# Optimization experiments

Measured on AMD Instinct MI355X. Metric: run time of the kernel, lower is better.

## Reference

```python
import jax, jax.numpy as jnp
import numpy as np

N_USER = 100000
N_ITEM = 50000
N = N_USER + N_ITEM  # 150000 nodes
D = 64               # embedding_size
L = 3                # num_layers
E = 2000000          # edges
B = 8192             # batch of (user, item_p, item_n) triples
INT_W, POP_W, TIDE_W = 0.1, 0.1, 0.2


def setup_inputs() -> dict:
    key = jax.random.key(0)
    ks = jax.random.split(key, 10)
    stdv = 1.0 / np.sqrt(D)
    emb_int = jax.random.uniform(ks[0], (N, D), minval=-stdv, maxval=stdv, dtype=jnp.float32)
    emb_pop = jax.random.uniform(ks[1], (N, D), minval=-stdv, maxval=stdv, dtype=jnp.float32)
    q = jax.random.uniform(ks[2], (N_ITEM,), dtype=jnp.float32)
    b = jax.random.uniform(ks[3], (N_ITEM,), dtype=jnp.float32)
    user = jax.random.randint(ks[4], (B, 1), 0, N_USER)
    item_p = jax.random.randint(ks[5], (B, 1), 0, N_ITEM)
    item_n = jax.random.randint(ks[6], (B, 1), 0, N_ITEM)
    mask = jax.random.randint(ks[7], (B, 1), 0, 2).astype(bool)
    edge_src = jax.random.randint(ks[8], (E,), 0, N)
    edge_dst = jax.random.randint(ks[9], (E,), 0, N)
    return {"emb_int": emb_int, "emb_pop": emb_pop, "q": q, "b": b,
            "user": user, "item_p": item_p, "item_n": item_n, "mask": mask,
            "edge_src": edge_src, "edge_dst": edge_dst}


def reference(emb_int, emb_pop, q, b, user, item_p, item_n, mask, edge_src, edge_dst):
    # --- LightGCN symmetric normalization coefficients (per edge) ---
    ones = jnp.ones(edge_src.shape, emb_int.dtype)
    deg_out = jax.ops.segment_sum(ones, edge_src, num_segments=N)
    deg_in = jax.ops.segment_sum(ones, edge_dst, num_segments=N)
    norm = (jax.lax.rsqrt(jnp.maximum(deg_out, 1.0))[edge_src]
            * jax.lax.rsqrt(jnp.maximum(deg_in, 1.0))[edge_dst])  # [E]

    def propagate(e0):
        # L layers of LGConv (gather-scale-scatter), mean over layer outputs incl. layer 0.
        # Dropout is identity in eval mode (training=False).
        acc, h = e0, e0
        for _ in range(L):
            h = jax.ops.segment_sum(h[edge_src] * norm[:, None], edge_dst, num_segments=N)
            acc = acc + h
        return acc / (L + 1)

    f_int = propagate(emb_int)  # [N, D]
    f_pop = propagate(emb_pop)  # [N, D]

    ip = item_p + N_USER  # item node ids
    inn = item_n + N_USER
    u_i, u_p = f_int[user], f_pop[user]          # [B, 1, D]
    pi_i, pi_p = f_int[ip], f_pop[ip]
    ni_i, ni_p = f_int[inn], f_pop[inn]

    p_score_int = jnp.sum(u_i * pi_i, axis=2)    # [B, 1]
    n_score_int = jnp.sum(u_i * ni_i, axis=2)
    p_score_pop = jnp.sum(u_p * pi_p, axis=2)
    n_score_pop = jnp.sum(u_p * ni_p, axis=2)
    p_score_total = p_score_int + p_score_pop
    n_score_total = n_score_int + n_score_pop

    mf = mask.astype(p_score_int.dtype)
    nmf = (~mask).astype(p_score_int.dtype)

    def mask_bpr(p, n, m):
        return -jnp.mean(m * jax.nn.log_sigmoid(p - n))

    def bpr(p, n):
        return -jnp.mean(jax.nn.log_sigmoid(p - n))

    loss_int = mask_bpr(p_score_int, n_score_int, mf)
    loss_pop = mask_bpr(n_score_pop, p_score_pop, mf) - mask_bpr(p_score_pop, n_score_pop, nmf)

    pop_p = jax.nn.softplus(q[item_p]) + jax.nn.softplus(b[item_p])  # [B, 1]
    pop_n = jax.nn.softplus(q[item_n]) + jax.nn.softplus(b[item_n])
    loss_tide = bpr(jnp.tanh(pop_p) * p_score_total, jnp.tanh(pop_n) * n_score_total)

    return INT_W * loss_int + POP_W * loss_pop + TIDE_W * loss_tide
```

## Files before the change

kernel.cpp:

```cpp
#include <hip/hip_runtime.h>
#include <hip/hip_bf16.h>
#include <math.h>

#define N_USER 100000
#define N_ITEM 50000
#define NNODE  150000
#define DIM    64
#define NEDGE  2000000
#define BSZ    8192
#define NTGT   (3*BSZ)
#define CB     586
#define NB     512
#define CH     ((NEDGE + NB - 1)/NB)
#define LBLK   2048
#define PREPB  (NNODE*32/256)
#define CAP    5120

typedef float v2f __attribute__((ext_vector_type(2)));

__device__ __forceinline__ float logsigf(float x){
    return fminf(x, 0.f) - log1pf(expf(-fabsf(x)));
}
__device__ __forceinline__ float softplusf(float x){
    return fmaxf(x, 0.f) + log1pf(expf(-fabsf(x)));
}
__device__ __forceinline__ v2f fp8x2_to_f32(unsigned short u){
    return __builtin_amdgcn_cvt_pk_f32_fp8((int)u, false);
}
__device__ __forceinline__ unsigned short f32_to_fp8x2(float a, float b){
    return (unsigned short)__builtin_amdgcn_cvt_pk_fp8_f32(a, b, 0, false);
}
__device__ __forceinline__ unsigned rfl(unsigned v){
    return (unsigned)__builtin_amdgcn_readfirstlane((int)v);
}

__device__ __forceinline__ void scanCB(unsigned* arr, unsigned* tmp){
    int t = threadIdx.x;
    int base = 3*t;
    unsigned a0=0,a1=0,a2=0;
    if(base   < CB) a0 = arr[base];
    if(base+1 < CB) a1 = arr[base+1];
    if(base+2 < CB) a2 = arr[base+2];
    unsigned s = a0+a1+a2;
    tmp[t]=s; __syncthreads();
    for(int off=1; off<256; off<<=1){
        unsigned v = (t>=off)? tmp[t-off] : 0u;
        __syncthreads();
        tmp[t] += v;
        __syncthreads();
    }
    unsigned excl = tmp[t]-s;
    if(base   < CB) arr[base]   = excl;
    if(base+1 < CB) arr[base+1] = excl+a0;
    if(base+2 < CB) arr[base+2] = excl+a0+a1;
    __syncthreads();
}

__global__ __launch_bounds__(256) void k_hist(const int* __restrict__ src, const int* __restrict__ dst,
                       unsigned* __restrict__ histD, unsigned* __restrict__ histS,
                       const float2* __restrict__ ei, const float2* __restrict__ ep,
                       unsigned* __restrict__ hC32,
                       const unsigned char* __restrict__ mask8, unsigned* __restrict__ mflag){
    if(blockIdx.x >= NB){
        if(blockIdx.x == NB + PREPB){
            __shared__ int any;
            if(threadIdx.x==0) any=0;
            __syncthreads();
            for(int i=threadIdx.x;i<BSZ;i+=256){ if((i&3) && mask8[i]) any=1; }
            __syncthreads();
            if(threadIdx.x==0) *mflag = (any!=0) ? 1u : 0u;
            return;
        }
        int idx = (blockIdx.x - NB)*256 + threadIdx.x;
        int n = idx>>5, c = idx&31;
        float2 va, vb;
        if(c<16){ va = ei[(size_t)n*32 + 2*c]; vb = ei[(size_t)n*32 + 2*c+1]; }
        else    { va = ep[(size_t)n*32 + 2*c-32]; vb = ep[(size_t)n*32 + 2*c-31]; }
        int d = __builtin_amdgcn_cvt_pk_fp8_f32(va.x, va.y, 0, false);
        d = __builtin_amdgcn_cvt_pk_fp8_f32(vb.x, vb.y, d, true);
        hC32[(size_t)n*32 + c] = (unsigned)d;
        return;
    }
    __shared__ unsigned hD[CB], hS[CB];
    for(int i=threadIdx.x;i<CB;i+=256){ hD[i]=0; hS[i]=0; }
    __syncthreads();
    int lo = blockIdx.x*CH, hi = min(lo+CH, NEDGE);
    for(int e=lo+threadIdx.x; e<hi; e+=256){
        atomicAdd(&hS[src[e]>>8],1u);
        atomicAdd(&hD[dst[e]>>8],1u);
    }
    __syncthreads();
    for(int i=threadIdx.x;i<CB;i+=256){
        histD[(size_t)blockIdx.x*CB + i]=hD[i];
        histS[(size_t)blockIdx.x*CB + i]=hS[i];
    }
}

__global__ __launch_bounds__(512) void k_colscan(unsigned* __restrict__ histD, unsigned* __restrict__ histS,
                          unsigned* __restrict__ ctD, unsigned* __restrict__ ctS){
    unsigned* hist = blockIdx.y ? histS : histD;
    unsigned* ct   = blockIdx.y ? ctS   : ctD;
    int b = blockIdx.x;
    __shared__ unsigned sh[512];
    unsigned v = hist[(size_t)threadIdx.x*CB + b];
    sh[threadIdx.x] = v;
    __syncthreads();
    for(int off=1; off<512; off<<=1){
        unsigned t = (threadIdx.x>=off)? sh[threadIdx.x-off] : 0u;
        __syncthreads();
        sh[threadIdx.x] += t;
        __syncthreads();
    }
    hist[(size_t)threadIdx.x*CB + b] = sh[threadIdx.x] - v;
    if(threadIdx.x==511) ct[b] = sh[511];
}

__global__ __launch_bounds__(1024) void k_bstart(const unsigned* __restrict__ ctD, const unsigned* __restrict__ ctS,
                         unsigned* __restrict__ bsD, unsigned* __restrict__ bsS){
    __shared__ unsigned sh[1024];
    unsigned v = (threadIdx.x<CB)? ctD[threadIdx.x] : 0u;
    sh[threadIdx.x]=v; __syncthreads();
    for(int off=1; off<1024; off<<=1){ unsigned t=(threadIdx.x>=off)?sh[threadIdx.x-off]:0u; __syncthreads(); sh[threadIdx.x]+=t; __syncthreads(); }
    if(threadIdx.x<CB) bsD[threadIdx.x]=sh[threadIdx.x]-v;
    if(threadIdx.x==CB-1) bsD[CB]=sh[threadIdx.x];
    __syncthreads();
    unsigned v2 = (threadIdx.x<CB)? ctS[threadIdx.x] : 0u;
    sh[threadIdx.x]=v2; __syncthreads();
    for(int off=1; off<1024; off<<=1){ unsigned t=(threadIdx.x>=off)?sh[threadIdx.x-off]:0u; __syncthreads(); sh[threadIdx.x]+=t; __syncthreads(); }
    if(threadIdx.x<CB) bsS[threadIdx.x]=sh[threadIdx.x]-v2;
    if(threadIdx.x==CB-1) bsS[CB]=sh[threadIdx.x];
}

__global__ __launch_bounds__(256) void k_scatter(const int* __restrict__ src, const int* __restrict__ dst,
                          const unsigned* __restrict__ histD, const unsigned* __restrict__ histS,
                          const unsigned* __restrict__ bsD, const unsigned* __restrict__ bsS,
                          unsigned* __restrict__ part, unsigned char* __restrict__ spart){
    __shared__ unsigned curD[CB], curS[CB];
    __shared__ unsigned lhD[CB], lhS[CB];
    __shared__ unsigned startD[CB], startS[CB];
    __shared__ unsigned tmp[256];
    __shared__ unsigned partl[CH];
    __shared__ unsigned short keyD[CH];
    __shared__ unsigned short keyS[CH];
    __shared__ unsigned char sl[CH];
    for(int i=threadIdx.x;i<CB;i+=256){
        curD[i]=bsD[i]+histD[(size_t)blockIdx.x*CB+i];
        curS[i]=bsS[i]+histS[(size_t)blockIdx.x*CB+i];
        lhD[i]=0; lhS[i]=0;
    }
    __syncthreads();
    int lo=blockIdx.x*CH, hi=min(lo+CH,NEDGE);
    int n = hi-lo;
    for(int e=lo+threadIdx.x;e<hi;e+=256){
        atomicAdd(&lhD[dst[e]>>8],1u);
        atomicAdd(&lhS[src[e]>>8],1u);
    }
    __syncthreads();
    scanCB(lhD, tmp);
    scanCB(lhS, tmp);
    for(int i=threadIdx.x;i<CB;i+=256){ startD[i]=lhD[i]; startS[i]=lhS[i]; }
    __syncthreads();
    for(int e=lo+threadIdx.x;e<hi;e+=256){
        int s=src[e], d=dst[e];
        unsigned bd=(unsigned)(d>>8);
        unsigned slot=atomicAdd(&lhD[bd],1u);
        partl[slot]=((unsigned)(d&255)<<18)|(unsigned)s;
        keyD[slot]=(unsigned short)bd;
        unsigned bs=(unsigned)(s>>8);
        unsigned sslot=atomicAdd(&lhS[bs],1u);
        sl[sslot]=(unsigned char)(s&255);
        keyS[sslot]=(unsigned short)bs;
    }
    __syncthreads();
    for(int k=threadIdx.x;k<n;k+=256){
        unsigned b=keyD[k];
        part[curD[b] + (unsigned)k - startD[b]] = partl[k];
    }
    for(int k=threadIdx.x;k<n;k+=256){
        unsigned b=keyS[k];
        spart[curS[b] + (unsigned)k - startS[b]] = sl[k];
    }
}

__global__ __launch_bounds__(256) void k_degO(const unsigned char* __restrict__ spart, const unsigned* __restrict__ bsS,
                       float* __restrict__ rsqO){
    __shared__ unsigned cnt[256];
    cnt[threadIdx.x]=0;
    __syncthreads();
    unsigned lo=bsS[blockIdx.x], hi=bsS[blockIdx.x+1];
    for(unsigned e=lo+threadIdx.x;e<hi;e+=256) atomicAdd(&cnt[spart[e]],1u);
    __syncthreads();
    int node=(blockIdx.x<<8)+(int)threadIdx.x;
    if(node<NNODE) rsqO[node]=rsqrtf(fmaxf((float)cnt[threadIdx.x],1.f));
}

__global__ __launch_bounds__(256) void k_csr(const unsigned* __restrict__ part, const unsigned* __restrict__ bsD,
                      const float* __restrict__ rsqO,
                      unsigned* __restrict__ rs, unsigned* __restrict__ degI,
                      unsigned* __restrict__ ec){
    __shared__ unsigned cnt[256], cur[256], sh[256];
    __shared__ float rsq[256];
    __shared__ unsigned partl[CAP];
    cnt[threadIdx.x]=0;
    __syncthreads();
    unsigned lo=bsD[blockIdx.x], hi=bsD[blockIdx.x+1];
    unsigned n = hi-lo;
    for(unsigned e=lo+threadIdx.x;e<hi;e+=256) atomicAdd(&cnt[part[e]>>18],1u);
    __syncthreads();
    unsigned c=cnt[threadIdx.x];
    sh[threadIdx.x]=c; __syncthreads();
    for(int o=1;o<256;o<<=1){ unsigned t=(threadIdx.x>=o)?sh[threadIdx.x-o]:0u; __syncthreads(); sh[threadIdx.x]+=t; __syncthreads(); }
    unsigned ex = sh[threadIdx.x]-c;
    rsq[threadIdx.x]=rsqrtf(fmaxf((float)c,1.f));
    cur[threadIdx.x]=ex;
    int node=(blockIdx.x<<8)+(int)threadIdx.x;
    if(node<NNODE){ degI[node]=c; rs[node]=lo+ex; }
    __syncthreads();
    if(n <= CAP){
        for(unsigned e=lo+threadIdx.x;e<hi;e+=256){
            unsigned p=part[e];
            unsigned slot=atomicAdd(&cur[p>>18],1u);
            partl[slot]=p;
        }
        __syncthreads();
        for(unsigned k=threadIdx.x;k<n;k+=256){
            unsigned p=partl[k];
            unsigned fb=p>>18, s=p&0x3FFFFu;
            float w=rsq[fb]*rsqO[s];
            unsigned w14=(unsigned)(w*16383.f + 0.5f);
            ec[lo+k]=(w14<<18)|s;
        }
    } else {
        for(unsigned e=lo+threadIdx.x;e<hi;e+=256){
            unsigned p=part[e];
            unsigned fb=p>>18, s=p&0x3FFFFu;
            unsigned pos=lo+atomicAdd(&cur[fb],1u);
            float w=rsq[fb]*rsqO[s];
            unsigned w14=(unsigned)(w*16383.f + 0.5f);
            ec[pos]=(w14<<18)|s;
        }
    }
}

__device__ __forceinline__ void drain_row(const unsigned short* __restrict__ hin,
                                          const unsigned* __restrict__ ec,
                                          unsigned s, unsigned c, unsigned &i, int lane,
                                          float &ax, float &ay){
    for(; i+4<=c; i+=4){
        unsigned e0=__builtin_nontemporal_load(&ec[s+i]);
        unsigned e1=__builtin_nontemporal_load(&ec[s+i+1]);
        unsigned e2=__builtin_nontemporal_load(&ec[s+i+2]);
        unsigned e3=__builtin_nontemporal_load(&ec[s+i+3]);
        unsigned short u0=hin[(size_t)(e0&0x3FFFFu)*64+lane];
        unsigned short u1=hin[(size_t)(e1&0x3FFFFu)*64+lane];
        unsigned short u2=hin[(size_t)(e2&0x3FFFFu)*64+lane];
        unsigned short u3=hin[(size_t)(e3&0x3FFFFu)*64+lane];
        float w0=(float)(e0>>18)*(1.f/16383.f), w1=(float)(e1>>18)*(1.f/16383.f);
        float w2=(float)(e2>>18)*(1.f/16383.f), w3=(float)(e3>>18)*(1.f/16383.f);
        v2f v;
        v=fp8x2_to_f32(u0); ax+=w0*v.x; ay+=w0*v.y;
        v=fp8x2_to_f32(u1); ax+=w1*v.x; ay+=w1*v.y;
        v=fp8x2_to_f32(u2); ax+=w2*v.x; ay+=w2*v.y;
        v=fp8x2_to_f32(u3); ax+=w3*v.x; ay+=w3*v.y;
    }
    for(; i<c; ++i){
        unsigned e0=__builtin_nontemporal_load(&ec[s+i]);
        unsigned short u0=hin[(size_t)(e0&0x3FFFFu)*64+lane];
        float w0=(float)(e0>>18)*(1.f/16383.f);
        v2f v=fp8x2_to_f32(u0); ax+=w0*v.x; ay+=w0*v.y;
    }
}

__global__ __launch_bounds__(256) void k_spmm_c(const unsigned short* __restrict__ hin, unsigned short* __restrict__ hout,
                                                const unsigned* __restrict__ rs, const unsigned* __restrict__ degI,
                                                const unsigned* __restrict__ ec){
    int wv = (blockIdx.x*256 + threadIdx.x) >> 6;
    int lane = threadIdx.x & 63;
    int r = 4*wv;
    if(r >= NNODE) return;
    unsigned s0=rfl(rs[r  ]), c0=rfl(degI[r  ]);
    unsigned s1=rfl(rs[r+1]), c1=rfl(degI[r+1]);
    unsigned s2=rfl(rs[r+2]), c2=rfl(degI[r+2]);
    unsigned s3=rfl(rs[r+3]), c3=rfl(degI[r+3]);
    float ax0=0,ay0=0, ax1=0,ay1=0, ax2=0,ay2=0, ax3=0,ay3=0;
    unsigned i0=0,i1=0,i2=0,i3=0;
    while(i0+4<=c0 && i1+4<=c1 && i2+4<=c2 && i3+4<=c3){
        unsigned e00=__builtin_nontemporal_load(&ec[s0+i0]);
        unsigned e01=__builtin_nontemporal_load(&ec[s0+i0+1]);
        unsigned e02=__builtin_nontemporal_load(&ec[s0+i0+2]);
        unsigned e03=__builtin_nontemporal_load(&ec[s0+i0+3]);
        unsigned e10=__builtin_nontemporal_load(&ec[s1+i1]);
        unsigned e11=__builtin_nontemporal_load(&ec[s1+i1+1]);
        unsigned e12=__builtin_nontemporal_load(&ec[s1+i1+2]);
        unsigned e13=__builtin_nontemporal_load(&ec[s1+i1+3]);
        unsigned e20=__builtin_nontemporal_load(&ec[s2+i2]);
        unsigned e21=__builtin_nontemporal_load(&ec[s2+i2+1]);
        unsigned e22=__builtin_nontemporal_load(&ec[s2+i2+2]);
        unsigned e23=__builtin_nontemporal_load(&ec[s2+i2+3]);
        unsigned e30=__builtin_nontemporal_load(&ec[s3+i3]);
        unsigned e31=__builtin_nontemporal_load(&ec[s3+i3+1]);
        unsigned e32=__builtin_nontemporal_load(&ec[s3+i3+2]);
        unsigned e33=__builtin_nontemporal_load(&ec[s3+i3+3]);
        unsigned short u00=hin[(size_t)(e00&0x3FFFFu)*64+lane];
        unsigned short u01=hin[(size_t)(e01&0x3FFFFu)*64+lane];
        unsigned short u02=hin[(size_t)(e02&0x3FFFFu)*64+lane];
        unsigned short u03=hin[(size_t)(e03&0x3FFFFu)*64+lane];
        unsigned short u10=hin[(size_t)(e10&0x3FFFFu)*64+lane];
        unsigned short u11=hin[(size_t)(e11&0x3FFFFu)*64+lane];
        unsigned short u12=hin[(size_t)(e12&0x3FFFFu)*64+lane];
        unsigned short u13=hin[(size_t)(e13&0x3FFFFu)*64+lane];
        unsigned short u20=hin[(size_t)(e20&0x3FFFFu)*64+lane];
        unsigned short u21=hin[(size_t)(e21&0x3FFFFu)*64+lane];
        unsigned short u22=hin[(size_t)(e22&0x3FFFFu)*64+lane];
        unsigned short u23=hin[(size_t)(e23&0x3FFFFu)*64+lane];
        unsigned short u30=hin[(size_t)(e30&0x3FFFFu)*64+lane];
        unsigned short u31=hin[(size_t)(e31&0x3FFFFu)*64+lane];
        unsigned short u32v=hin[(size_t)(e32&0x3FFFFu)*64+lane];
        unsigned short u33=hin[(size_t)(e33&0x3FFFFu)*64+lane];
        v2f v; float w;
        v=fp8x2_to_f32(u00); w=(float)(e00>>18)*(1.f/16383.f); ax0+=w*v.x; ay0+=w*v.y;
        v=fp8x2_to_f32(u01); w=(float)(e01>>18)*(1.f/16383.f); ax0+=w*v.x; ay0+=w*v.y;
        v=fp8x2_to_f32(u02); w=(float)(e02>>18)*(1.f/16383.f); ax0+=w*v.x; ay0+=w*v.y;
        v=fp8x2_to_f32(u03); w=(float)(e03>>18)*(1.f/16383.f); ax0+=w*v.x; ay0+=w*v.y;
        v=fp8x2_to_f32(u10); w=(float)(e10>>18)*(1.f/16383.f); ax1+=w*v.x; ay1+=w*v.y;
        v=fp8x2_to_f32(u11); w=(float)(e11>>18)*(1.f/16383.f); ax1+=w*v.x; ay1+=w*v.y;
        v=fp8x2_to_f32(u12); w=(float)(e12>>18)*(1.f/16383.f); ax1+=w*v.x; ay1+=w*v.y;
        v=fp8x2_to_f32(u13); w=(float)(e13>>18)*(1.f/16383.f); ax1+=w*v.x; ay1+=w*v.y;
        v=fp8x2_to_f32(u20); w=(float)(e20>>18)*(1.f/16383.f); ax2+=w*v.x; ay2+=w*v.y;
        v=fp8x2_to_f32(u21); w=(float)(e21>>18)*(1.f/16383.f); ax2+=w*v.x; ay2+=w*v.y;
        v=fp8x2_to_f32(u22); w=(float)(e22>>18)*(1.f/16383.f); ax2+=w*v.x; ay2+=w*v.y;
        v=fp8x2_to_f32(u23); w=(float)(e23>>18)*(1.f/16383.f); ax2+=w*v.x; ay2+=w*v.y;
        v=fp8x2_to_f32(u30); w=(float)(e30>>18)*(1.f/16383.f); ax3+=w*v.x; ay3+=w*v.y;
        v=fp8x2_to_f32(u31); w=(float)(e31>>18)*(1.f/16383.f); ax3+=w*v.x; ay3+=w*v.y;
        v=fp8x2_to_f32(u32v); w=(float)(e32>>18)*(1.f/16383.f); ax3+=w*v.x; ay3+=w*v.y;
        v=fp8x2_to_f32(u33); w=(float)(e33>>18)*(1.f/16383.f); ax3+=w*v.x; ay3+=w*v.y;
        i0+=4; i1+=4; i2+=4; i3+=4;
    }
    drain_row(hin, ec, s0, c0, i0, lane, ax0, ay0);
    drain_row(hin, ec, s1, c1, i1, lane, ax1, ay1);
    drain_row(hin, ec, s2, c2, i2, lane, ax2, ay2);
    drain_row(hin, ec, s3, c3, i3, lane, ax3, ay3);
    hout[(size_t)(r  )*64+lane] = f32_to_fp8x2(ax0, ay0);
    hout[(size_t)(r+1)*64+lane] = f32_to_fp8x2(ax1, ay1);
    hout[(size_t)(r+2)*64+lane] = f32_to_fp8x2(ax2, ay2);
    hout[(size_t)(r+3)*64+lane] = f32_to_fp8x2(ax3, ay3);
}

__global__ __launch_bounds__(256) void k_spmm_t(const unsigned short* __restrict__ hin, float2* __restrict__ h3,
                                                const unsigned* __restrict__ rs, const unsigned* __restrict__ degI,
                                                const unsigned* __restrict__ ec,
                                                const int* __restrict__ user, const int* __restrict__ itp,
                                                const int* __restrict__ itn){
    int wv = (blockIdx.x*256 + threadIdx.x) >> 6;
    int lane = threadIdx.x & 63;
    int t0 = 2*wv, t1 = 2*wv+1;
    if(t0 >= NTGT) return;
    int sec0 = t0>>13, b0 = t0&(BSZ-1);
    int sec1 = t1>>13, b1 = t1&(BSZ-1);
    int n0 = (sec0==0) ? user[b0] : ((sec0==1) ? itp[b0]+N_USER : itn[b0]+N_USER);
    int n1 = (sec1==0) ? user[b1] : ((sec1==1) ? itp[b1]+N_USER : itn[b1]+N_USER);
    n0 = __builtin_amdgcn_readfirstlane(n0);
    n1 = __builtin_amdgcn_readfirstlane(n1);
    unsigned s0 = rfl(rs[n0]), c0 = rfl(degI[n0]);
    unsigned s1 = rfl(rs[n1]), c1 = rfl(degI[n1]);
    float ax0=0.f, ay0=0.f, ax1=0.f, ay1=0.f;
    unsigned i0=0, i1=0;
    while(i0+4<=c0 && i1+4<=c1){
        unsigned e0=ec[s0+i0], e1=ec[s0+i0+1], e2=ec[s0+i0+2], e3=ec[s0+i0+3];
        unsigned e4=ec[s1+i1], e5=ec[s1+i1+1], e6=ec[s1+i1+2], e7=ec[s1+i1+3];
        unsigned short u0=hin[(size_t)(e0&0x3FFFFu)*64+lane];
        unsigned short u1=hin[(size_t)(e1&0x3FFFFu)*64+lane];
        unsigned short u2=hin[(size_t)(e2&0x3FFFFu)*64+lane];
        unsigned short u3=hin[(size_t)(e3&0x3FFFFu)*64+lane];
        unsigned short u4=hin[(size_t)(e4&0x3FFFFu)*64+lane];
        unsigned short u5=hin[(size_t)(e5&0x3FFFFu)*64+lane];
        unsigned short u6=hin[(size_t)(e6&0x3FFFFu)*64+lane];
        unsigned short u7=hin[(size_t)(e7&0x3FFFFu)*64+lane];
        float w0=(float)(e0>>18)*(1.f/16383.f), w1=(float)(e1>>18)*(1.f/16383.f);
        float w2=(float)(e2>>18)*(1.f/16383.f), w3=(float)(e3>>18)*(1.f/16383.f);
        float w4=(float)(e4>>18)*(1.f/16383.f), w5=(float)(e5>>18)*(1.f/16383.f);
        float w6=(float)(e6>>18)*(1.f/16383.f), w7=(float)(e7>>18)*(1.f/16383.f);
        v2f v;
        v=fp8x2_to_f32(u0); ax0+=w0*v.x; ay0+=w0*v.y;
        v=fp8x2_to_f32(u1); ax0+=w1*v.x; ay0+=w1*v.y;
        v=fp8x2_to_f32(u2); ax0+=w2*v.x; ay0+=w2*v.y;
        v=fp8x2_to_f32(u3); ax0+=w3*v.x; ay0+=w3*v.y;
        v=fp8x2_to_f32(u4); ax1+=w4*v.x; ay1+=w4*v.y;
        v=fp8x2_to_f32(u5); ax1+=w5*v.x; ay1+=w5*v.y;
        v=fp8x2_to_f32(u6); ax1+=w6*v.x; ay1+=w6*v.y;
        v=fp8x2_to_f32(u7); ax1+=w7*v.x; ay1+=w7*v.y;
        i0+=4; i1+=4;
    }
    drain_row(hin, ec, s0, c0, i0, lane, ax0, ay0);
    drain_row(hin, ec, s1, c1, i1, lane, ax1, ay1);
    h3[(size_t)t0*64+lane] = make_float2(ax0, ay0);
    h3[(size_t)t1*64+lane] = make_float2(ax1, ay1);
}

__global__ __launch_bounds__(256) void k_scoreloss(const float2* __restrict__ ei, const float2* __restrict__ ep,
                        const unsigned short* __restrict__ h1C, const unsigned short* __restrict__ h2C,
                        const float2* __restrict__ h3,
                        const float* __restrict__ q, const float* __restrict__ bq,
                        const int* __restrict__ user, const int* __restrict__ item_p, const int* __restrict__ item_n,
                        const void* __restrict__ mask, const unsigned* __restrict__ mflag,
                        float4* __restrict__ partial){
    int t = blockIdx.x*256 + threadIdx.x;
    int b = t >> 6, l = t & 63;
    int wv = threadIdx.x >> 6;
    __shared__ float4 wsum[4];
    int nu = user[b];
    int np = item_p[b] + N_USER;
    int nn = item_n[b] + N_USER;

    float2 e0u, e0p, e0n;
    if(l < 32){
        e0u = ei[(size_t)nu*32 + l]; e0p = ei[(size_t)np*32 + l]; e0n = ei[(size_t)nn*32 + l];
    } else {
        e0u = ep[(size_t)nu*32 + (l-32)]; e0p = ep[(size_t)np*32 + (l-32)]; e0n = ep[(size_t)nn*32 + (l-32)];
    }
    v2f h1u = fp8x2_to_f32(h1C[(size_t)nu*64 + l]);
    v2f h1p = fp8x2_to_f32(h1C[(size_t)np*64 + l]);
    v2f h1n = fp8x2_to_f32(h1C[(size_t)nn*64 + l]);
    v2f h2u = fp8x2_to_f32(h2C[(size_t)nu*64 + l]);
    v2f h2p = fp8x2_to_f32(h2C[(size_t)np*64 + l]);
    v2f h2n = fp8x2_to_f32(h2C[(size_t)nn*64 + l]);
    float2 h3u = h3[(size_t)b*64 + l];
    float2 h3p = h3[(size_t)(BSZ   + b)*64 + l];
    float2 h3n = h3[(size_t)(2*BSZ + b)*64 + l];

    float fux = e0u.x + h1u.x + h2u.x + h3u.x, fuy = e0u.y + h1u.y + h2u.y + h3u.y;
    float fpx = e0p.x + h1p.x + h2p.x + h3p.x, fpy = e0p.y + h1p.y + h2p.y + h3p.y;
    float fnx = e0n.x + h1n.x + h2n.x + h3n.x, fny = e0n.y + h1n.y + h2n.y + h3n.y;

    float dp = fux*fpx + fuy*fpy;
    float dn = fux*fnx + fuy*fny;
    for(int off=16; off; off>>=1){ dp += __shfl_down(dp,off,32); dn += __shfl_down(dn,off,32); }
    float pi  = __shfl(dp, 0, 64) * (1.f/16.f);
    float ni  = __shfl(dn, 0, 64) * (1.f/16.f);
    float pp  = __shfl(dp, 32, 64) * (1.f/16.f);
    float npp = __shfl(dn, 32, 64) * (1.f/16.f);
    if(l == 0){
        bool bytes = (*mflag)!=0;
        float mf = bytes ? (((const unsigned char*)mask)[b]?1.f:0.f)
                         : (((const int*)mask)[b]?1.f:0.f);
        float nmf = 1.f-mf;
        float a0 = mf  * logsigf(pi-ni);
        float a1 = mf  * logsigf(npp-pp);
        float a2 = nmf * logsigf(pp-npp);
        int ip=item_p[b], in_=item_n[b];
        float popp = softplusf(q[ip]) + softplusf(bq[ip]);
        float popn = softplusf(q[in_]) + softplusf(bq[in_]);
        float a3 = logsigf(tanhf(popp)*(pi+pp) - tanhf(popn)*(ni+npp));
        wsum[wv] = make_float4(a0,a1,a2,a3);
    }
    __syncthreads();
    if(threadIdx.x == 0){
        float4 s0=wsum[0], s1=wsum[1], s2=wsum[2], s3=wsum[3];
        partial[blockIdx.x] = make_float4(s0.x+s1.x+s2.x+s3.x, s0.y+s1.y+s2.y+s3.y,
                                          s0.z+s1.z+s2.z+s3.z, s0.w+s1.w+s2.w+s3.w);
    }
}

__global__ __launch_bounds__(256) void k_lossfin(const float4* __restrict__ partial, float* __restrict__ out){
    __shared__ float4 sh[256];
    float4 s = make_float4(0,0,0,0);
    for(int i=threadIdx.x; i<LBLK; i+=256){
        float4 v = partial[i];
        s.x+=v.x; s.y+=v.y; s.z+=v.z; s.w+=v.w;
    }
    sh[threadIdx.x]=s;
    __syncthreads();
    for(int off=128; off; off>>=1){
        if(threadIdx.x < off){
            float4 a=sh[threadIdx.x], b2=sh[threadIdx.x+off];
            sh[threadIdx.x]=make_float4(a.x+b2.x,a.y+b2.y,a.z+b2.z,a.w+b2.w);
        }
        __syncthreads();
    }
    if(threadIdx.x==0){
        const float invB = 1.f/(float)BSZ;
        float4 t = sh[0];
        float loss_int  = -t.x*invB;
        float loss_pop  = -t.y*invB + t.z*invB;
        float loss_tide = -t.w*invB;
        out[0] = 0.1f*loss_int + 0.1f*loss_pop + 0.2f*loss_tide;
    }
}

extern "C" void kernel_launch(void* const* d_in, const int* in_sizes, int n_in,
                              void* d_out, int out_size, void* d_ws, size_t ws_size,
                              hipStream_t stream){
    const float* emb_int = (const float*)d_in[0];
    const float* emb_pop = (const float*)d_in[1];
    const float* q    = (const float*)d_in[2];
    const float* bq   = (const float*)d_in[3];
    const int* user   = (const int*)d_in[4];
    const int* item_p = (const int*)d_in[5];
    const int* item_n = (const int*)d_in[6];
    const void* mask  = d_in[7];
    const int* esrc   = (const int*)d_in[8];
    const int* edst   = (const int*)d_in[9];

    char* ws = (char*)d_ws;
    size_t o = 0;
    auto take = [&](size_t bytes)->char*{ char* p = ws + o; o = (o + bytes + 255) & ~(size_t)255; return p; };
    unsigned* histD = (unsigned*)take((size_t)NB*CB*4);
    unsigned* histS = (unsigned*)take((size_t)NB*CB*4);
    unsigned* ctD   = (unsigned*)take((size_t)CB*4);
    unsigned* ctS   = (unsigned*)take((size_t)CB*4);
    unsigned* bsD   = (unsigned*)take((size_t)(CB+1)*4);
    unsigned* bsS   = (unsigned*)take((size_t)(CB+1)*4);
    unsigned* part  = (unsigned*)take((size_t)NEDGE*4);
    unsigned char* spart = (unsigned char*)take((size_t)NEDGE);
    float*    rsqO  = (float*)take((size_t)NNODE*4);
    unsigned* degI  = (unsigned*)take((size_t)NNODE*4);
    unsigned* rs    = (unsigned*)take((size_t)NNODE*4);
    unsigned* ec    = (unsigned*)take((size_t)NEDGE*4);
    unsigned short* hE  = (unsigned short*)take((size_t)NNODE*64*2);
    unsigned short* h1C = (unsigned short*)take((size_t)NNODE*64*2);
    unsigned short* h2C = (unsigned short*)take((size_t)NNODE*64*2);
    float2*   h3    = (float2*)take((size_t)NTGT*64*8);
    float4*   partial = (float4*)take((size_t)LBLK*16);
    unsigned* mflag = (unsigned*)take(256);
    (void)ws_size; (void)in_sizes; (void)n_in; (void)out_size;

    k_hist<<<NB + PREPB + 1,256,0,stream>>>(esrc, edst, histD, histS,
                                            (const float2*)emb_int, (const float2*)emb_pop,
                                            (unsigned*)hE, (const unsigned char*)mask, mflag);
    k_colscan<<<dim3(CB,2),512,0,stream>>>(histD, histS, ctD, ctS);
    k_bstart<<<1,1024,0,stream>>>(ctD, ctS, bsD, bsS);
    k_scatter<<<NB,256,0,stream>>>(esrc, edst, histD, histS, bsD, bsS, part, spart);
    k_degO<<<CB,256,0,stream>>>(spart, bsS, rsqO);
    k_csr<<<CB,256,0,stream>>>(part, bsD, rsqO, rs, degI, ec);

    const int spB = ((NNODE/4)*64 + 255)/256;
    k_spmm_c<<<spB,256,0,stream>>>(hE,  h1C, rs, degI, ec);
    k_spmm_c<<<spB,256,0,stream>>>(h1C, h2C, rs, degI, ec);
    k_spmm_t<<<((NTGT/2)*64 + 255)/256,256,0,stream>>>(h2C, h3, rs, degI, ec,
                                                 user, item_p, item_n);
    k_scoreloss<<<LBLK,256,0,stream>>>((const float2*)emb_int, (const float2*)emb_pop,
                                       h1C, h2C, h3, q, bq, user, item_p, item_n,
                                       mask, mflag, partial);
    k_lossfin<<<1,256,0,stream>>>(partial, (float*)d_out);
}
```

Baseline: 356.1 us.

## Factor edge norm into per-node scales and drop per-edge weights from SpMM

Rewrites the LightGCN normalization so each layer stores features pre-scaled by rsqrt of the source's out-degree. The SpMM becomes an unweighted sum of gathered fp8 rows, followed by a single per-row scale. Out-degree is now counted with global atomics, which removes the whole source-side partition, scan and degO kernels. Edge entries hold precomputed byte offsets into a padded feature table whose zero row at index 0 lets the loops skip bounds checks, with buffer loads covering out-of-range edges. The trade-off is changed fp8 quantization scaling and higher global atomic contention in the histogram pass.

```diff
diff --git a/kernel.cpp b/kernel.cpp
--- a/kernel.cpp
+++ b/kernel.cpp
@@ -16,6 +16,15 @@
 #define PREPB  (NNODE*32/256)
 #define CAP    5120
 
+#ifndef __has_builtin
+#define __has_builtin(x) 0
+#endif
+#if __has_builtin(__builtin_amdgcn_make_buffer_rsrc) && __has_builtin(__builtin_amdgcn_raw_buffer_load_b32)
+#define USE_BUF 1
+#else
+#define USE_BUF 0
+#endif
+
 typedef float v2f __attribute__((ext_vector_type(2)));
 
 __device__ __forceinline__ float logsigf(float x){
@@ -33,6 +42,22 @@
 __device__ __forceinline__ unsigned rfl(unsigned v){
     return (unsigned)__builtin_amdgcn_readfirstlane((int)v);
 }
+__device__ __forceinline__ unsigned umax2(unsigned a, unsigned b){ return a>b ? a : b; }
+
+#if USE_BUF
+typedef __amdgpu_buffer_rsrc_t rsrc_t;
+__device__ __forceinline__ rsrc_t mkrsrc(const unsigned* p, unsigned bytes){
+    return __builtin_amdgcn_make_buffer_rsrc((void*)p, (short)0, (int)bytes, 0x00020000);
+}
+__device__ __forceinline__ unsigned bload(rsrc_t r, int voff, int soff){
+    return (unsigned)__builtin_amdgcn_raw_buffer_load_b32(r, voff, soff, 0);
+}
+#define DEF_ROW(J) rsrc_t R##J = mkrsrc(ec + s##J, c##J*4u);
+#define LOADE(J,K,i) bload(R##J, 4*(K), (int)(4u*(i)))
+#else
+#define DEF_ROW(J)
+#define LOADE(J,K,i) ((((i)+(K)) < c##J) ? __builtin_nontemporal_load(&ec[s##J + (i) + (K)]) : 0u)
+#endif
 
 __device__ __forceinline__ void scanCB(unsigned* arr, unsigned* tmp){
     int t = threadIdx.x;
@@ -57,52 +82,34 @@
 }
 
 __global__ __launch_bounds__(256) void k_hist(const int* __restrict__ src, const int* __restrict__ dst,
-                       unsigned* __restrict__ histD, unsigned* __restrict__ histS,
-                       const float2* __restrict__ ei, const float2* __restrict__ ep,
-                       unsigned* __restrict__ hC32,
+                       unsigned* __restrict__ histD, unsigned* __restrict__ degO,
                        const unsigned char* __restrict__ mask8, unsigned* __restrict__ mflag){
-    if(blockIdx.x >= NB){
-        if(blockIdx.x == NB + PREPB){
-            __shared__ int any;
-            if(threadIdx.x==0) any=0;
-            __syncthreads();
-            for(int i=threadIdx.x;i<BSZ;i+=256){ if((i&3) && mask8[i]) any=1; }
-            __syncthreads();
-            if(threadIdx.x==0) *mflag = (any!=0) ? 1u : 0u;
-            return;
-        }
-        int idx = (blockIdx.x - NB)*256 + threadIdx.x;
-        int n = idx>>5, c = idx&31;
-        float2 va, vb;
-        if(c<16){ va = ei[(size_t)n*32 + 2*c]; vb = ei[(size_t)n*32 + 2*c+1]; }
-        else    { va = ep[(size_t)n*32 + 2*c-32]; vb = ep[(size_t)n*32 + 2*c-31]; }
-        int d = __builtin_amdgcn_cvt_pk_fp8_f32(va.x, va.y, 0, false);
-        d = __builtin_amdgcn_cvt_pk_fp8_f32(vb.x, vb.y, d, true);
-        hC32[(size_t)n*32 + c] = (unsigned)d;
+    if(blockIdx.x == NB){
+        __shared__ int any;
+        if(threadIdx.x==0) any=0;
+        __syncthreads();
+        for(int i=threadIdx.x;i<BSZ;i+=256){ if((i&3) && mask8[i]) any=1; }
+        __syncthreads();
+        if(threadIdx.x==0) *mflag = (any!=0) ? 1u : 0u;
         return;
     }
-    __shared__ unsigned hD[CB], hS[CB];
-    for(int i=threadIdx.x;i<CB;i+=256){ hD[i]=0; hS[i]=0; }
+    __shared__ unsigned hD[CB];
+    for(int i=threadIdx.x;i<CB;i+=256) hD[i]=0;
     __syncthreads();
     int lo = blockIdx.x*CH, hi = min(lo+CH, NEDGE);
     for(int e=lo+threadIdx.x; e<hi; e+=256){
-        atomicAdd(&hS[src[e]>>8],1u);
         atomicAdd(&hD[dst[e]>>8],1u);
-    }
-    __syncthreads();
-    for(int i=threadIdx.x;i<CB;i+=256){
+        atomicAdd(&degO[src[e]],1u);
+    }
+    __syncthreads();
+    for(int i=threadIdx.x;i<CB;i+=256)
         histD[(size_t)blockIdx.x*CB + i]=hD[i];
-        histS[(size_t)blockIdx.x*CB + i]=hS[i];
-    }
-}
-
-__global__ __launch_bounds__(512) void k_colscan(unsigned* __restrict__ histD, unsigned* __restrict__ histS,
-                          unsigned* __restrict__ ctD, unsigned* __restrict__ ctS){
-    unsigned* hist = blockIdx.y ? histS : histD;
-    unsigned* ct   = blockIdx.y ? ctS   : ctD;
+}
+
+__global__ __launch_bounds__(512) void k_colscan(unsigned* __restrict__ histD, unsigned* __restrict__ ctD){
     int b = blockIdx.x;
     __shared__ unsigned sh[512];
-    unsigned v = hist[(size_t)threadIdx.x*CB + b];
+    unsigned v = histD[(size_t)threadIdx.x*CB + b];
     sh[threadIdx.x] = v;
     __syncthreads();
     for(int off=1; off<512; off<<=1){
@@ -111,54 +118,63 @@
         sh[threadIdx.x] += t;
         __syncthreads();
     }
-    hist[(size_t)threadIdx.x*CB + b] = sh[threadIdx.x] - v;
-    if(threadIdx.x==511) ct[b] = sh[511];
-}
-
-__global__ __launch_bounds__(1024) void k_bstart(const unsigned* __restrict__ ctD, const unsigned* __restrict__ ctS,
-                         unsigned* __restrict__ bsD, unsigned* __restrict__ bsS){
+    histD[(size_t)threadIdx.x*CB + b] = sh[threadIdx.x] - v;
+    if(threadIdx.x==511) ctD[b] = sh[511];
+}
+
+__global__ __launch_bounds__(1024) void k_bstart(const unsigned* __restrict__ ctD, unsigned* __restrict__ bsD){
     __shared__ unsigned sh[1024];
     unsigned v = (threadIdx.x<CB)? ctD[threadIdx.x] : 0u;
     sh[threadIdx.x]=v; __syncthreads();
     for(int off=1; off<1024; off<<=1){ unsigned t=(threadIdx.x>=off)?sh[threadIdx.x-off]:0u; __syncthreads(); sh[threadIdx.x]+=t; __syncthreads(); }
     if(threadIdx.x<CB) bsD[threadIdx.x]=sh[threadIdx.x]-v;
     if(threadIdx.x==CB-1) bsD[CB]=sh[threadIdx.x];
-    __syncthreads();
-    unsigned v2 = (threadIdx.x<CB)? ctS[threadIdx.x] : 0u;
-    sh[threadIdx.x]=v2; __syncthreads();
-    for(int off=1; off<1024; off<<=1){ unsigned t=(threadIdx.x>=off)?sh[threadIdx.x-off]:0u; __syncthreads(); sh[threadIdx.x]+=t; __syncthreads(); }
-    if(threadIdx.x<CB) bsS[threadIdx.x]=sh[threadIdx.x]-v2;
-    if(threadIdx.x==CB-1) bsS[CB]=sh[threadIdx.x];
+}
+
+__global__ __launch_bounds__(256) void k_prep(const float2* __restrict__ ei, const float2* __restrict__ ep,
+                      const unsigned* __restrict__ degO,
+                      unsigned* __restrict__ hE32, unsigned* __restrict__ h1g, unsigned* __restrict__ h2g,
+                      unsigned* __restrict__ ecpad, float* __restrict__ sqd){
+    if(blockIdx.x == PREPB){
+        int t = threadIdx.x;
+        if(t < 32) hE32[t] = 0u;
+        else if(t < 64) h1g[t-32] = 0u;
+        else if(t < 96) h2g[t-64] = 0u;
+        else if(t < 160) ecpad[t-96] = 0u;
+        return;
+    }
+    int idx = blockIdx.x*256 + threadIdx.x;
+    int n = idx>>5, c = idx&31;
+    float dv = fmaxf((float)degO[n], 1.f);
+    float sc = 8.f*rsqrtf(dv);
+    float2 va, vb;
+    if(c<16){ va = ei[(size_t)n*32 + 2*c]; vb = ei[(size_t)n*32 + 2*c+1]; }
+    else    { va = ep[(size_t)n*32 + 2*c-32]; vb = ep[(size_t)n*32 + 2*c-31]; }
+    int d = __builtin_amdgcn_cvt_pk_fp8_f32(va.x*sc, va.y*sc, 0, false);
+    d = __builtin_amdgcn_cvt_pk_fp8_f32(vb.x*sc, vb.y*sc, d, true);
+    hE32[32 + (size_t)n*32 + c] = (unsigned)d;
+    if(c==0) sqd[n] = sqrtf(dv)*0.125f;
 }
 
 __global__ __launch_bounds__(256) void k_scatter(const int* __restrict__ src, const int* __restrict__ dst,
-                          const unsigned* __restrict__ histD, const unsigned* __restrict__ histS,
-                          const unsigned* __restrict__ bsD, const unsigned* __restrict__ bsS,
-                          unsigned* __restrict__ part, unsigned char* __restrict__ spart){
-    __shared__ unsigned curD[CB], curS[CB];
-    __shared__ unsigned lhD[CB], lhS[CB];
-    __shared__ unsigned startD[CB], startS[CB];
+                          const unsigned* __restrict__ histD, const unsigned* __restrict__ bsD,
+                          unsigned* __restrict__ part){
+    __shared__ unsigned curD[CB], lhD[CB], startD[CB];
     __shared__ unsigned tmp[256];
     __shared__ unsigned partl[CH];
     __shared__ unsigned short keyD[CH];
-    __shared__ unsigned short keyS[CH];
-    __shared__ unsigned char sl[CH];
     for(int i=threadIdx.x;i<CB;i+=256){
         curD[i]=bsD[i]+histD[(size_t)blockIdx.x*CB+i];
-        curS[i]=bsS[i]+histS[(size_t)blockIdx.x*CB+i];
-        lhD[i]=0; lhS[i]=0;
+        lhD[i]=0;
     }
     __syncthreads();
     int lo=blockIdx.x*CH, hi=min(lo+CH,NEDGE);
     int n = hi-lo;
-    for(int e=lo+threadIdx.x;e<hi;e+=256){
+    for(int e=lo+threadIdx.x;e<hi;e+=256)
         atomicAdd(&lhD[dst[e]>>8],1u);
-        atomicAdd(&lhS[src[e]>>8],1u);
-    }
     __syncthreads();
     scanCB(lhD, tmp);
-    scanCB(lhS, tmp);
-    for(int i=threadIdx.x;i<CB;i+=256){ startD[i]=lhD[i]; startS[i]=lhS[i]; }
+    for(int i=threadIdx.x;i<CB;i+=256) startD[i]=lhD[i];
     __syncthreads();
     for(int e=lo+threadIdx.x;e<hi;e+=256){
         int s=src[e], d=dst[e];
@@ -166,40 +182,19 @@
         unsigned slot=atomicAdd(&lhD[bd],1u);
         partl[slot]=((unsigned)(d&255)<<18)|(unsigned)s;
         keyD[slot]=(unsigned short)bd;
-        unsigned bs=(unsigned)(s>>8);
-        unsigned sslot=atomicAdd(&lhS[bs],1u);
-        sl[sslot]=(unsigned char)(s&255);
-        keyS[sslot]=(unsigned short)bs;
     }
     __syncthreads();
     for(int k=threadIdx.x;k<n;k+=256){
         unsigned b=keyD[k];
         part[curD[b] + (unsigned)k - startD[b]] = partl[k];
     }
-    for(int k=threadIdx.x;k<n;k+=256){
-        unsigned b=keyS[k];
-        spart[curS[b] + (unsigned)k - startS[b]] = sl[k];
-    }
-}
-
-__global__ __launch_bounds__(256) void k_degO(const unsigned char* __restrict__ spart, const unsigned* __restrict__ bsS,
-                       float* __restrict__ rsqO){
-    __shared__ unsigned cnt[256];
-    cnt[threadIdx.x]=0;
-    __syncthreads();
-    unsigned lo=bsS[blockIdx.x], hi=bsS[blockIdx.x+1];
-    for(unsigned e=lo+threadIdx.x;e<hi;e+=256) atomicAdd(&cnt[spart[e]],1u);
-    __syncthreads();
-    int node=(blockIdx.x<<8)+(int)threadIdx.x;
-    if(node<NNODE) rsqO[node]=rsqrtf(fmaxf((float)cnt[threadIdx.x],1.f));
 }
 
 __global__ __launch_bounds__(256) void k_csr(const unsigned* __restrict__ part, const unsigned* __restrict__ bsD,
-                      const float* __restrict__ rsqO,
+                      const unsigned* __restrict__ degO,
                       unsigned* __restrict__ rs, unsigned* __restrict__ degI,
-                      unsigned* __restrict__ ec){
+                      unsigned* __restrict__ ec, float* __restrict__ srow, float* __restrict__ rsqI8){
     __shared__ unsigned cnt[256], cur[256], sh[256];
-    __shared__ float rsq[256];
     __shared__ unsigned partl[CAP];
     cnt[threadIdx.x]=0;
     __syncthreads();
@@ -211,10 +206,15 @@
     sh[threadIdx.x]=c; __syncthreads();
     for(int o=1;o<256;o<<=1){ unsigned t=(threadIdx.x>=o)?sh[threadIdx.x-o]:0u; __syncthreads(); sh[threadIdx.x]+=t; __syncthreads(); }
     unsigned ex = sh[threadIdx.x]-c;
-    rsq[threadIdx.x]=rsqrtf(fmaxf((float)c,1.f));
     cur[threadIdx.x]=ex;
     int node=(blockIdx.x<<8)+(int)threadIdx.x;
-    if(node<NNODE){ degI[node]=c; rs[node]=lo+ex; }
+    if(node<NNODE){
+        degI[node]=c; rs[node]=lo+ex;
+        float rI = rsqrtf(fmaxf((float)c,1.f));
+        float rO = rsqrtf(fmaxf((float)degO[node],1.f));
+        srow[node]  = rI*rO;
+        rsqI8[node] = rI*0.125f;
+    }
     __syncthreads();
     if(n <= CAP){
         for(unsigned e=lo+threadIdx.x;e<hi;e+=256){
@@ -225,55 +225,20 @@
         __syncthreads();
         for(unsigned k=threadIdx.x;k<n;k+=256){
             unsigned p=partl[k];
-            unsigned fb=p>>18, s=p&0x3FFFFu;
-            float w=rsq[fb]*rsqO[s];
-            unsigned w14=(unsigned)(w*16383.f + 0.5f);
-            ec[lo+k]=(w14<<18)|s;
+            ec[lo+k] = ((p&0x3FFFFu)+1u)<<7;
         }
     } else {
         for(unsigned e=lo+threadIdx.x;e<hi;e+=256){
             unsigned p=part[e];
-            unsigned fb=p>>18, s=p&0x3FFFFu;
-            unsigned pos=lo+atomicAdd(&cur[fb],1u);
-            float w=rsq[fb]*rsqO[s];
-            unsigned w14=(unsigned)(w*16383.f + 0.5f);
-            ec[pos]=(w14<<18)|s;
+            unsigned pos=lo+atomicAdd(&cur[p>>18],1u);
+            ec[pos] = ((p&0x3FFFFu)+1u)<<7;
         }
     }
 }
 
-__device__ __forceinline__ void drain_row(const unsigned short* __restrict__ hin,
-                                          const unsigned* __restrict__ ec,
-                                          unsigned s, unsigned c, unsigned &i, int lane,
-                                          float &ax, float &ay){
-    for(; i+4<=c; i+=4){
-        unsigned e0=__builtin_nontemporal_load(&ec[s+i]);
-        unsigned e1=__builtin_nontemporal_load(&ec[s+i+1]);
-        unsigned e2=__builtin_nontemporal_load(&ec[s+i+2]);
-        unsigned e3=__builtin_nontemporal_load(&ec[s+i+3]);
-        unsigned short u0=hin[(size_t)(e0&0x3FFFFu)*64+lane];
-        unsigned short u1=hin[(size_t)(e1&0x3FFFFu)*64+lane];
-        unsigned short u2=hin[(size_t)(e2&0x3FFFFu)*64+lane];
-        unsigned short u3=hin[(size_t)(e3&0x3FFFFu)*64+lane];
-        float w0=(float)(e0>>18)*(1.f/16383.f), w1=(float)(e1>>18)*(1.f/16383.f);
-        float w2=(float)(e2>>18)*(1.f/16383.f), w3=(float)(e3>>18)*(1.f/16383.f);
-        v2f v;
-        v=fp8x2_to_f32(u0); ax+=w0*v.x; ay+=w0*v.y;
-        v=fp8x2_to_f32(u1); ax+=w1*v.x; ay+=w1*v.y;
-        v=fp8x2_to_f32(u2); ax+=w2*v.x; ay+=w2*v.y;
-        v=fp8x2_to_f32(u3); ax+=w3*v.x; ay+=w3*v.y;
-    }
-    for(; i<c; ++i){
-        unsigned e0=__builtin_nontemporal_load(&ec[s+i]);
-        unsigned short u0=hin[(size_t)(e0&0x3FFFFu)*64+lane];
-        float w0=(float)(e0>>18)*(1.f/16383.f);
-        v2f v=fp8x2_to_f32(u0); ax+=w0*v.x; ay+=w0*v.y;
-    }
-}
-
-__global__ __launch_bounds__(256) void k_spmm_c(const unsigned short* __restrict__ hin, unsigned short* __restrict__ hout,
+__global__ __launch_bounds__(256) void k_spmm_c(const unsigned short* __restrict__ hinb, unsigned short* __restrict__ houtb,
                                                 const unsigned* __restrict__ rs, const unsigned* __restrict__ degI,
-                                                const unsigned* __restrict__ ec){
+                                                const unsigned* __restrict__ ec, const float* __restrict__ srow){
     int wv = (blockIdx.x*256 + threadIdx.x) >> 6;
     int lane = threadIdx.x & 63;
     int r = 4*wv;
@@ -282,73 +247,47 @@
     unsigned s1=rfl(rs[r+1]), c1=rfl(degI[r+1]);
     unsigned s2=rfl(rs[r+2]), c2=rfl(degI[r+2]);
     unsigned s3=rfl(rs[r+3]), c3=rfl(degI[r+3]);
-    float ax0=0,ay0=0, ax1=0,ay1=0, ax2=0,ay2=0, ax3=0,ay3=0;
-    unsigned i0=0,i1=0,i2=0,i3=0;
-    while(i0+4<=c0 && i1+4<=c1 && i2+4<=c2 && i3+4<=c3){
-        unsigned e00=__builtin_nontemporal_load(&ec[s0+i0]);
-        unsigned e01=__builtin_nontemporal_load(&ec[s0+i0+1]);
-        unsigned e02=__builtin_nontemporal_load(&ec[s0+i0+2]);
-        unsigned e03=__builtin_nontemporal_load(&ec[s0+i0+3]);
-        unsigned e10=__builtin_nontemporal_load(&ec[s1+i1]);
-        unsigned e11=__builtin_nontemporal_load(&ec[s1+i1+1]);
-        unsigned e12=__builtin_nontemporal_load(&ec[s1+i1+2]);
-        unsigned e13=__builtin_nontemporal_load(&ec[s1+i1+3]);
-        unsigned e20=__builtin_nontemporal_load(&ec[s2+i2]);
-        unsigned e21=__builtin_nontemporal_load(&ec[s2+i2+1]);
-        unsigned e22=__builtin_nontemporal_load(&ec[s2+i2+2]);
-        unsigned e23=__builtin_nontemporal_load(&ec[s2+i2+3]);
-        unsigned e30=__builtin_nontemporal_load(&ec[s3+i3]);
-        unsigned e31=__builtin_nontemporal_load(&ec[s3+i3+1]);
-        unsigned e32=__builtin_nontemporal_load(&ec[s3+i3+2]);
-        unsigned e33=__builtin_nontemporal_load(&ec[s3+i3+3]);
-        unsigned short u00=hin[(size_t)(e00&0x3FFFFu)*64+lane];
-        unsigned short u01=hin[(size_t)(e01&0x3FFFFu)*64+lane];
-        unsigned short u02=hin[(size_t)(e02&0x3FFFFu)*64+lane];
-        unsigned short u03=hin[(size_t)(e03&0x3FFFFu)*64+lane];
-        unsigned short u10=hin[(size_t)(e10&0x3FFFFu)*64+lane];
-        unsigned short u11=hin[(size_t)(e11&0x3FFFFu)*64+lane];
-        unsigned short u12=hin[(size_t)(e12&0x3FFFFu)*64+lane];
-        unsigned short u13=hin[(size_t)(e13&0x3FFFFu)*64+lane];
-        unsigned short u20=hin[(size_t)(e20&0x3FFFFu)*64+lane];
-        unsigned short u21=hin[(size_t)(e21&0x3FFFFu)*64+lane];
-        unsigned short u22=hin[(size_t)(e22&0x3FFFFu)*64+lane];
-        unsigned short u23=hin[(size_t)(e23&0x3FFFFu)*64+lane];
-        unsigned short u30=hin[(size_t)(e30&0x3FFFFu)*64+lane];
-        unsigned short u31=hin[(size_t)(e31&0x3FFFFu)*64+lane];
-        unsigned short u32v=hin[(size_t)(e32&0x3FFFFu)*64+lane];
-        unsigned short u33=hin[(size_t)(e33&0x3FFFFu)*64+lane];
-        v2f v; float w;
-        v=fp8x2_to_f32(u00); w=(float)(e00>>18)*(1.f/16383.f); ax0+=w*v.x; ay0+=w*v.y;
-        v=fp8x2_to_f32(u01); w=(float)(e01>>18)*(1.f/16383.f); ax0+=w*v.x; ay0+=w*v.y;
-        v=fp8x2_to_f32(u02); w=(float)(e02>>18)*(1.f/16383.f); ax0+=w*v.x; ay0+=w*v.y;
-        v=fp8x2_to_f32(u03); w=(float)(e03>>18)*(1.f/16383.f); ax0+=w*v.x; ay0+=w*v.y;
-        v=fp8x2_to_f32(u10); w=(float)(e10>>18)*(1.f/16383.f); ax1+=w*v.x; ay1+=w*v.y;
-        v=fp8x2_to_f32(u11); w=(float)(e11>>18)*(1.f/16383.f); ax1+=w*v.x; ay1+=w*v.y;
-        v=fp8x2_to_f32(u12); w=(float)(e12>>18)*(1.f/16383.f); ax1+=w*v.x; ay1+=w*v.y;
-        v=fp8x2_to_f32(u13); w=(float)(e13>>18)*(1.f/16383.f); ax1+=w*v.x; ay1+=w*v.y;
-        v=fp8x2_to_f32(u20); w=(float)(e20>>18)*(1.f/16383.f); ax2+=w*v.x; ay2+=w*v.y;
-        v=fp8x2_to_f32(u21); w=(float)(e21>>18)*(1.f/16383.f); ax2+=w*v.x; ay2+=w*v.y;
-        v=fp8x2_to_f32(u22); w=(float)(e22>>18)*(1.f/16383.f); ax2+=w*v.x; ay2+=w*v.y;
-        v=fp8x2_to_f32(u23); w=(float)(e23>>18)*(1.f/16383.f); ax2+=w*v.x; ay2+=w*v.y;
-        v=fp8x2_to_f32(u30); w=(float)(e30>>18)*(1.f/16383.f); ax3+=w*v.x; ay3+=w*v.y;
-        v=fp8x2_to_f32(u31); w=(float)(e31>>18)*(1.f/16383.f); ax3+=w*v.x; ay3+=w*v.y;
-        v=fp8x2_to_f32(u32v); w=(float)(e32>>18)*(1.f/16383.f); ax3+=w*v.x; ay3+=w*v.y;
-        v=fp8x2_to_f32(u33); w=(float)(e33>>18)*(1.f/16383.f); ax3+=w*v.x; ay3+=w*v.y;
-        i0+=4; i1+=4; i2+=4; i3+=4;
-    }
-    drain_row(hin, ec, s0, c0, i0, lane, ax0, ay0);
-    drain_row(hin, ec, s1, c1, i1, lane, ax1, ay1);
-    drain_row(hin, ec, s2, c2, i2, lane, ax2, ay2);
-    drain_row(hin, ec, s3, c3, i3, lane, ax3, ay3);
-    hout[(size_t)(r  )*64+lane] = f32_to_fp8x2(ax0, ay0);
-    hout[(size_t)(r+1)*64+lane] = f32_to_fp8x2(ax1, ay1);
-    hout[(size_t)(r+2)*64+lane] = f32_to_fp8x2(ax2, ay2);
-    hout[(size_t)(r+3)*64+lane] = f32_to_fp8x2(ax3, ay3);
-}
-
-__global__ __launch_bounds__(256) void k_spmm_t(const unsigned short* __restrict__ hin, float2* __restrict__ h3,
+    DEF_ROW(0) DEF_ROW(1) DEF_ROW(2) DEF_ROW(3)
+    const char* hb = (const char*)hinb;
+    unsigned lane2 = ((unsigned)lane)*2u;
+    v2f a0={0.f,0.f}, a1={0.f,0.f}, a2={0.f,0.f}, a3={0.f,0.f};
+    unsigned cmax = umax2(umax2(c0,c1), umax2(c2,c3));
+    for(unsigned i=0; i<cmax; i+=4){
+        unsigned eA0=LOADE(0,0,i), eA1=LOADE(0,1,i), eA2=LOADE(0,2,i), eA3=LOADE(0,3,i);
+        unsigned eB0=LOADE(1,0,i), eB1=LOADE(1,1,i), eB2=LOADE(1,2,i), eB3=LOADE(1,3,i);
+        unsigned eC0=LOADE(2,0,i), eC1=LOADE(2,1,i), eC2=LOADE(2,2,i), eC3=LOADE(2,3,i);
+        unsigned eD0=LOADE(3,0,i), eD1=LOADE(3,1,i), eD2=LOADE(3,2,i), eD3=LOADE(3,3,i);
+        unsigned short uA0=*(const unsigned short*)(hb+eA0+lane2);
+        unsigned short uA1=*(const unsigned short*)(hb+eA1+lane2);
+        unsigned short uA2=*(const unsigned short*)(hb+eA2+lane2);
+        unsigned short uA3=*(const unsigned short*)(hb+eA3+lane2);
+        unsigned short uB0=*(const unsigned short*)(hb+eB0+lane2);
+        unsigned short uB1=*(const unsigned short*)(hb+eB1+lane2);
+        unsigned short uB2=*(const unsigned short*)(hb+eB2+lane2);
+        unsigned short uB3=*(const unsigned short*)(hb+eB3+lane2);
+        unsigned short uC0=*(const unsigned short*)(hb+eC0+lane2);
+        unsigned short uC1=*(const unsigned short*)(hb+eC1+lane2);
+        unsigned short uC2=*(const unsigned short*)(hb+eC2+lane2);
+        unsigned short uC3=*(const unsigned short*)(hb+eC3+lane2);
+        unsigned short uD0=*(const unsigned short*)(hb+eD0+lane2);
+        unsigned short uD1=*(const unsigned short*)(hb+eD1+lane2);
+        unsigned short uD2=*(const unsigned short*)(hb+eD2+lane2);
+        unsigned short uD3=*(const unsigned short*)(hb+eD3+lane2);
+        a0 += fp8x2_to_f32(uA0); a0 += fp8x2_to_f32(uA1); a0 += fp8x2_to_f32(uA2); a0 += fp8x2_to_f32(uA3);
+        a1 += fp8x2_to_f32(uB0); a1 += fp8x2_to_f32(uB1); a1 += fp8x2_to_f32(uB2); a1 += fp8x2_to_f32(uB3);
+        a2 += fp8x2_to_f32(uC0); a2 += fp8x2_to_f32(uC1); a2 += fp8x2_to_f32(uC2); a2 += fp8x2_to_f32(uC3);
+        a3 += fp8x2_to_f32(uD0); a3 += fp8x2_to_f32(uD1); a3 += fp8x2_to_f32(uD2); a3 += fp8x2_to_f32(uD3);
+    }
+    float sc0=srow[r], sc1=srow[r+1], sc2=srow[r+2], sc3=srow[r+3];
+    houtb[(size_t)(r+1)*64+lane] = f32_to_fp8x2(sc0*a0.x, sc0*a0.y);
+    houtb[(size_t)(r+2)*64+lane] = f32_to_fp8x2(sc1*a1.x, sc1*a1.y);
+    houtb[(size_t)(r+3)*64+lane] = f32_to_fp8x2(sc2*a2.x, sc2*a2.y);
+    houtb[(size_t)(r+4)*64+lane] = f32_to_fp8x2(sc3*a3.x, sc3*a3.y);
+}
+
+__global__ __launch_bounds__(256) void k_spmm_t(const unsigned short* __restrict__ hinb, float2* __restrict__ h3,
                                                 const unsigned* __restrict__ rs, const unsigned* __restrict__ degI,
-                                                const unsigned* __restrict__ ec,
+                                                const unsigned* __restrict__ ec, const float* __restrict__ rsqI8,
                                                 const int* __restrict__ user, const int* __restrict__ itp,
                                                 const int* __restrict__ itn){
     int wv = (blockIdx.x*256 + threadIdx.x) >> 6;
@@ -363,38 +302,28 @@
     n1 = __builtin_amdgcn_readfirstlane(n1);
     unsigned s0 = rfl(rs[n0]), c0 = rfl(degI[n0]);
     unsigned s1 = rfl(rs[n1]), c1 = rfl(degI[n1]);
-    float ax0=0.f, ay0=0.f, ax1=0.f, ay1=0.f;
-    unsigned i0=0, i1=0;
-    while(i0+4<=c0 && i1+4<=c1){
-        unsigned e0=ec[s0+i0], e1=ec[s0+i0+1], e2=ec[s0+i0+2], e3=ec[s0+i0+3];
-        unsigned e4=ec[s1+i1], e5=ec[s1+i1+1], e6=ec[s1+i1+2], e7=ec[s1+i1+3];
-        unsigned short u0=hin[(size_t)(e0&0x3FFFFu)*64+lane];
-        unsigned short u1=hin[(size_t)(e1&0x3FFFFu)*64+lane];
-        unsigned short u2=hin[(size_t)(e2&0x3FFFFu)*64+lane];
-        unsigned short u3=hin[(size_t)(e3&0x3FFFFu)*64+lane];
-        unsigned short u4=hin[(size_t)(e4&0x3FFFFu)*64+lane];
-        unsigned short u5=hin[(size_t)(e5&0x3FFFFu)*64+lane];
-        unsigned short u6=hin[(size_t)(e6&0x3FFFFu)*64+lane];
-        unsigned short u7=hin[(size_t)(e7&0x3FFFFu)*64+lane];
-        float w0=(float)(e0>>18)*(1.f/16383.f), w1=(float)(e1>>18)*(1.f/16383.f);
-        float w2=(float)(e2>>18)*(1.f/16383.f), w3=(float)(e3>>18)*(1.f/16383.f);
-        float w4=(float)(e4>>18)*(1.f/16383.f), w5=(float)(e5>>18)*(1.f/16383.f);
-        float w6=(float)(e6>>18)*(1.f/16383.f), w7=(float)(e7>>18)*(1.f/16383.f);
-        v2f v;
-        v=fp8x2_to_f32(u0); ax0+=w0*v.x; ay0+=w0*v.y;
-        v=fp8x2_to_f32(u1); ax0+=w1*v.x; ay0+=w1*v.y;
-        v=fp8x2_to_f32(u2); ax0+=w2*v.x; ay0+=w2*v.y;
-        v=fp8x2_to_f32(u3); ax0+=w3*v.x; ay0+=w3*v.y;
-        v=fp8x2_to_f32(u4); ax1+=w4*v.x; ay1+=w4*v.y;
-        v=fp8x2_to_f32(u5); ax1+=w5*v.x; ay1+=w5*v.y;
-        v=fp8x2_to_f32(u6); ax1+=w6*v.x; ay1+=w6*v.y;
-        v=fp8x2_to_f32(u7); ax1+=w7*v.x; ay1+=w7*v.y;
-        i0+=4; i1+=4;
-    }
-    drain_row(hin, ec, s0, c0, i0, lane, ax0, ay0);
-    drain_row(hin, ec, s1, c1, i1, lane, ax1, ay1);
-    h3[(size_t)t0*64+lane] = make_float2(ax0, ay0);
-    h3[(size_t)t1*64+lane] = make_float2(ax1, ay1);
+    DEF_ROW(0) DEF_ROW(1)
+    const char* hb = (const char*)hinb;
+    unsigned lane2 = ((unsigned)lane)*2u;
+    v2f a0={0.f,0.f}, a1={0.f,0.f};
+    unsigned cmax = umax2(c0,c1);
+    for(unsigned i=0; i<cmax; i+=4){
+        unsigned eA0=LOADE(0,0,i), eA1=LOADE(0,1,i), eA2=LOADE(0,2,i), eA3=LOADE(0,3,i);
+        unsigned eB0=LOADE(1,0,i), eB1=LOADE(1,1,i), eB2=LOADE(1,2,i), eB3=LOADE(1,3,i);
+        unsigned short uA0=*(const unsigned short*)(hb+eA0+lane2);
+        unsigned short uA1=*(const unsigned short*)(hb+eA1+lane2);
+        unsigned short uA2=*(const unsigned short*)(hb+eA2+lane2);
+        unsigned short uA3=*(const unsigned short*)(hb+eA3+lane2);
+        unsigned short uB0=*(const unsigned short*)(hb+eB0+lane2);
+        unsigned short uB1=*(const unsigned short*)(hb+eB1+lane2);
+        unsigned short uB2=*(const unsigned short*)(hb+eB2+lane2);
+        unsigned short uB3=*(const unsigned short*)(hb+eB3+lane2);
+        a0 += fp8x2_to_f32(uA0); a0 += fp8x2_to_f32(uA1); a0 += fp8x2_to_f32(uA2); a0 += fp8x2_to_f32(uA3);
+        a1 += fp8x2_to_f32(uB0); a1 += fp8x2_to_f32(uB1); a1 += fp8x2_to_f32(uB2); a1 += fp8x2_to_f32(uB3);
+    }
+    float t0s = rsqI8[n0], t1s = rsqI8[n1];
+    h3[(size_t)t0*64+lane] = make_float2(a0.x*t0s, a0.y*t0s);
+    h3[(size_t)t1*64+lane] = make_float2(a1.x*t1s, a1.y*t1s);
 }
 
 __global__ __launch_bounds__(256) void k_scoreloss(const float2* __restrict__ ei, const float2* __restrict__ ep,
@@ -403,6 +332,7 @@
                         const float* __restrict__ q, const float* __restrict__ bq,
                         const int* __restrict__ user, const int* __restrict__ item_p, const int* __restrict__ item_n,
                         const void* __restrict__ mask, const unsigned* __restrict__ mflag,
+                        const float* __restrict__ sqd,
                         float4* __restrict__ partial){
     int t = blockIdx.x*256 + threadIdx.x;
     int b = t >> 6, l = t & 63;
@@ -418,19 +348,21 @@
     } else {
         e0u = ep[(size_t)nu*32 + (l-32)]; e0p = ep[(size_t)np*32 + (l-32)]; e0n = ep[(size_t)nn*32 + (l-32)];
     }
-    v2f h1u = fp8x2_to_f32(h1C[(size_t)nu*64 + l]);
-    v2f h1p = fp8x2_to_f32(h1C[(size_t)np*64 + l]);
-    v2f h1n = fp8x2_to_f32(h1C[(size_t)nn*64 + l]);
-    v2f h2u = fp8x2_to_f32(h2C[(size_t)nu*64 + l]);
-    v2f h2p = fp8x2_to_f32(h2C[(size_t)np*64 + l]);
-    v2f h2n = fp8x2_to_f32(h2C[(size_t)nn*64 + l]);
+    v2f h1u = fp8x2_to_f32(h1C[(size_t)(nu+1)*64 + l]);
+    v2f h1p = fp8x2_to_f32(h1C[(size_t)(np+1)*64 + l]);
+    v2f h1n = fp8x2_to_f32(h1C[(size_t)(nn+1)*64 + l]);
+    v2f h2u = fp8x2_to_f32(h2C[(size_t)(nu+1)*64 + l]);
+    v2f h2p = fp8x2_to_f32(h2C[(size_t)(np+1)*64 + l]);
+    v2f h2n = fp8x2_to_f32(h2C[(size_t)(nn+1)*64 + l]);
     float2 h3u = h3[(size_t)b*64 + l];
     float2 h3p = h3[(size_t)(BSZ   + b)*64 + l];
     float2 h3n = h3[(size_t)(2*BSZ + b)*64 + l];
 
-    float fux = e0u.x + h1u.x + h2u.x + h3u.x, fuy = e0u.y + h1u.y + h2u.y + h3u.y;
-    float fpx = e0p.x + h1p.x + h2p.x + h3p.x, fpy = e0p.y + h1p.y + h2p.y + h3p.y;
-    float fnx = e0n.x + h1n.x + h2n.x + h3n.x, fny = e0n.y + h1n.y + h2n.y + h3n.y;
+    float squ = sqd[nu], sqp = sqd[np], sqn = sqd[nn];
+
+    float fux = e0u.x + squ*(h1u.x + h2u.x) + h3u.x, fuy = e0u.y + squ*(h1u.y + h2u.y) + h3u.y;
+    float fpx = e0p.x + sqp*(h1p.x + h2p.x) + h3p.x, fpy = e0p.y + sqp*(h1p.y + h2p.y) + h3p.y;
+    float fnx = e0n.x + sqn*(h1n.x + h2n.x) + h3n.x, fny = e0n.y + sqn*(h1n.y + h2n.y) + h3n.y;
 
     float dp = fux*fpx + fuy*fpy;
     float dn = fux*fnx + fuy*fny;
@@ -505,41 +437,42 @@
     size_t o = 0;
     auto take = [&](size_t bytes)->char*{ char* p = ws + o; o = (o + bytes + 255) & ~(size_t)255; return p; };
     unsigned* histD = (unsigned*)take((size_t)NB*CB*4);
-    unsigned* histS = (unsigned*)take((size_t)NB*CB*4);
     unsigned* ctD   = (unsigned*)take((size_t)CB*4);
-    unsigned* ctS   = (unsigned*)take((size_t)CB*4);
     unsigned* bsD   = (unsigned*)take((size_t)(CB+1)*4);
-    unsigned* bsS   = (unsigned*)take((size_t)(CB+1)*4);
+    unsigned* degO  = (unsigned*)take((size_t)NNODE*4);
     unsigned* part  = (unsigned*)take((size_t)NEDGE*4);
-    unsigned char* spart = (unsigned char*)take((size_t)NEDGE);
-    float*    rsqO  = (float*)take((size_t)NNODE*4);
+    unsigned* rs    = (unsigned*)take((size_t)NNODE*4);
     unsigned* degI  = (unsigned*)take((size_t)NNODE*4);
-    unsigned* rs    = (unsigned*)take((size_t)NNODE*4);
-    unsigned* ec    = (unsigned*)take((size_t)NEDGE*4);
-    unsigned short* hE  = (unsigned short*)take((size_t)NNODE*64*2);
-    unsigned short* h1C = (unsigned short*)take((size_t)NNODE*64*2);
-    unsigned short* h2C = (unsigned short*)take((size_t)NNODE*64*2);
+    unsigned* ec    = (unsigned*)take((size_t)NEDGE*4 + 256);
+    float*    srow  = (float*)take((size_t)NNODE*4);
+    float*    rsqI8 = (float*)take((size_t)NNODE*4);
+    float*    sqd   = (float*)take((size_t)NNODE*4);
+    unsigned short* hEb  = (unsigned short*)take((size_t)(NNODE+1)*64*2);
+    unsigned short* h1Cb = (unsigned short*)take((size_t)(NNODE+1)*64*2);
+    unsigned short* h2Cb = (unsigned short*)take((size_t)(NNODE+1)*64*2);
     float2*   h3    = (float2*)take((size_t)NTGT*64*8);
     float4*   partial = (float4*)take((size_t)LBLK*16);
     unsigned* mflag = (unsigned*)take(256);
     (void)ws_size; (void)in_sizes; (void)n_in; (void)out_size;
 
-    k_hist<<<NB + PREPB + 1,256,0,stream>>>(esrc, edst, histD, histS,
-                                            (const float2*)emb_int, (const float2*)emb_pop,
-                                            (unsigned*)hE, (const unsigned char*)mask, mflag);
-    k_colscan<<<dim3(CB,2),512,0,stream>>>(histD, histS, ctD, ctS);
-    k_bstart<<<1,1024,0,stream>>>(ctD, ctS, bsD, bsS);
-    k_scatter<<<NB,256,0,stream>>>(esrc, edst, histD, histS, bsD, bsS, part, spart);
-    k_degO<<<CB,256,0,stream>>>(spart, bsS, rsqO);
-    k_csr<<<CB,256,0,stream>>>(part, bsD, rsqO, rs, degI, ec);
+    hipMemsetAsync(degO, 0, (size_t)NNODE*4, stream);
+    k_hist<<<NB+1,256,0,stream>>>(esrc, edst, histD, degO,
+                                  (const unsigned char*)mask, mflag);
+    k_colscan<<<CB,512,0,stream>>>(histD, ctD);
+    k_bstart<<<1,1024,0,stream>>>(ctD, bsD);
+    k_prep<<<PREPB+1,256,0,stream>>>((const float2*)emb_int, (const float2*)emb_pop, degO,
+                                     (unsigned*)hEb, (unsigned*)h1Cb, (unsigned*)h2Cb,
+                                     ec + NEDGE, sqd);
+    k_scatter<<<NB,256,0,stream>>>(esrc, edst, histD, bsD, part);
+    k_csr<<<CB,256,0,stream>>>(part, bsD, degO, rs, degI, ec, srow, rsqI8);
 
     const int spB = ((NNODE/4)*64 + 255)/256;
-    k_spmm_c<<<spB,256,0,stream>>>(hE,  h1C, rs, degI, ec);
-    k_spmm_c<<<spB,256,0,stream>>>(h1C, h2C, rs, degI, ec);
-    k_spmm_t<<<((NTGT/2)*64 + 255)/256,256,0,stream>>>(h2C, h3, rs, degI, ec,
+    k_spmm_c<<<spB,256,0,stream>>>(hEb,  h1Cb, rs, degI, ec, srow);
+    k_spmm_c<<<spB,256,0,stream>>>(h1Cb, h2Cb, rs, degI, ec, srow);
+    k_spmm_t<<<((NTGT/2)*64 + 255)/256,256,0,stream>>>(h2Cb, h3, rs, degI, ec, rsqI8,
                                                  user, item_p, item_n);
     k_scoreloss<<<LBLK,256,0,stream>>>((const float2*)emb_int, (const float2*)emb_pop,
-                                       h1C, h2C, h3, q, bq, user, item_p, item_n,
-                                       mask, mflag, partial);
+                                       h1Cb, h2Cb, h3, q, bq, user, item_p, item_n,
+                                       mask, mflag, sqd, partial);
     k_lossfin<<<1,256,0,stream>>>(partial, (float*)d_out);
 }
```

Measured after the change: 406.8 us. 1.14x slower.
